# Kernel tuning notes

Hardware: AMD Instinct MI355X
Metric: run time of the kernel (lower is better)

Reference implementation:

```python
import jax, jax.numpy as jnp
import numpy as np

DIM = 256


def setup_inputs() -> dict:
    key = jax.random.key(0)
    ks = jax.random.split(key, 10)
    d = DIM
    inp = {
        "agent": jax.random.normal(ks[0], (64, d), dtype=jnp.float32),
        "x": jax.random.normal(ks[1], (8, 4096, d), dtype=jnp.float32),
        # parameters (stored as [in, out]; y = x @ W + b)
        "W_qkv": jax.random.normal(ks[2], (d, 3 * d), dtype=jnp.float32) * (d ** -0.5),
        "b_qkv": jnp.zeros((3 * d,), dtype=jnp.float32),
        "W_agent": jax.random.normal(ks[3], (d, 2 * d), dtype=jnp.float32) * (d ** -0.5),
        "b_agent": jnp.zeros((2 * d,), dtype=jnp.float32),
        "W_fc1": jax.random.normal(ks[4], (d, d), dtype=jnp.float32) * (d ** -0.5),
        "b_fc1": jnp.zeros((d,), dtype=jnp.float32),
        "W_fc2": jax.random.normal(ks[5], (d, d), dtype=jnp.float32) * (d ** -0.5),
        "b_fc2": jnp.zeros((d,), dtype=jnp.float32),
    }
    return inp


def reference(agent, x, W_qkv, b_qkv, W_agent, b_agent, W_fc1, b_fc1, W_fc2, b_fc2):
    d = x.shape[-1]
    scale = d ** -0.5
    # qkv projection of tokens: [B,N,3d] -> q,k,v each [B,N,d]
    qkv = x @ W_qkv + b_qkv
    q, k, v = jnp.split(qkv, 3, axis=-1)
    # agent projection: [K,2d] -> q_agent,k_agent each [K,d]
    ag = agent @ W_agent + b_agent
    q_agent, k_agent = jnp.split(ag, 2, axis=-1)
    # stage 1: agents attend over tokens -> [B,K,N]
    attn1 = jax.nn.softmax(jnp.einsum('kd,bnd->bkn', q_agent, k) * scale, axis=-1)
    va = jnp.einsum('bkn,bnd->bkd', attn1, v)  # [B,K,d]
    va = va @ W_fc1 + b_fc1
    # stage 2: tokens attend over agents -> [B,N,K]
    attn2 = jax.nn.softmax(jnp.einsum('bnd,kd->bnk', q, k_agent) * scale, axis=-1)
    out = jnp.einsum('bnk,bkd->bnd', attn2, va)  # [B,N,d]
    out = out @ W_fc2 + b_fc2
    return out + x
```

## Files before the change

kernel.cpp:

```cpp
#include <hip/hip_runtime.h>
#include <stdint.h>
#include <string.h>

#define BB 8
#define NN 4096
#define DD 256
#define SCALE 0.0625f

using frag_ab = __attribute__((ext_vector_type(8))) short;
using frag_cd = __attribute__((ext_vector_type(4))) float;

__device__ __forceinline__ unsigned short f2bf(float f) {
    union { float f; unsigned u; } a; a.f = f;
    unsigned r = a.u + 0x7FFFu + ((a.u >> 16) & 1u);
    return (unsigned short)(r >> 16);
}

__global__ __launch_bounds__(256) void k_xprep(
    const float* __restrict__ x, unsigned short* __restrict__ xb,
    unsigned short* __restrict__ xt)
{
    __shared__ float T[64 * 65];
    const int n0 = blockIdx.x * 64, d0 = blockIdx.y * 64, b = blockIdx.z;
    const int tid = threadIdx.x;
#pragma unroll
    for (int p = 0; p < 16; ++p) {
        int idx = p * 256 + tid;
        int n = idx >> 6, d = idx & 63;
        T[n * 65 + d] = x[(size_t)(b * 4096 + n0 + n) * 256 + d0 + d];
    }
    __syncthreads();
#pragma unroll
    for (int p = 0; p < 16; ++p) {
        int idx = p * 256 + tid;
        int n = idx >> 6, d = idx & 63;
        xb[(size_t)(b * 4096 + n0 + n) * 256 + d0 + d] = f2bf(T[n * 65 + d]);
    }
#pragma unroll
    for (int p = 0; p < 16; ++p) {
        int idx = p * 256 + tid;
        int d = idx >> 6, n = idx & 63;
        xt[(size_t)(b * 256 + d0 + d) * 4096 + n0 + n] = f2bf(T[n * 65 + d]);
    }
}

__global__ __launch_bounds__(256) void k_setup1(
    const float* __restrict__ agent, const float* __restrict__ Wag,
    const float* __restrict__ bag, float* __restrict__ ag,
    const float* __restrict__ Wqkv, const float* __restrict__ Wfc1,
    const float* __restrict__ bqkv, const float* __restrict__ bfc1,
    float* __restrict__ T, float* __restrict__ Tb)
{
    __shared__ float sh[256];
    const int bx = blockIdx.x, tid = threadIdx.x;
    if (bx < 64) {
        sh[tid] = agent[bx * 256 + tid];
        __syncthreads();
#pragma unroll
        for (int h = 0; h < 2; ++h) {
            int j = tid + h * 256;
            float s = bag[j];
            for (int kk = 0; kk < 256; ++kk) s += sh[kk] * Wag[kk * 512 + j];
            ag[bx * 512 + j] = s;
        }
    } else {
        const int i = bx - 64;
        sh[tid] = Wqkv[i * 768 + 512 + tid];
        __syncthreads();
        float s = 0.f;
        for (int o = 0; o < 256; ++o) s += sh[o] * Wfc1[o * 256 + tid];
        T[i * 256 + tid] = s;
        if (i == 0) {
            float t = bfc1[tid];
            for (int o = 0; o < 256; ++o) t += bqkv[512 + o] * Wfc1[o * 256 + tid];
            Tb[tid] = t;
        }
    }
}

__global__ __launch_bounds__(256) void k_setup2(
    const float* __restrict__ ag, const float* __restrict__ Wqkv,
    const float* __restrict__ bqkv, unsigned short* __restrict__ P12t,
    float* __restrict__ c12, const float* __restrict__ T,
    const float* __restrict__ Tb, const float* __restrict__ Wfc2,
    float* __restrict__ W3, float* __restrict__ b3)
{
    __shared__ float arow[256];
    __shared__ float red[256];
    const int bx = blockIdx.x, tid = threadIdx.x;
    if (bx < 128) {
        const int c = bx;
        const int woff = (c < 64) ? 256 : 0;
        const int aoff = (c < 64) ? 0 : 256;
        const int row = c & 63;
        arow[tid] = ag[row * 512 + aoff + tid];
        __syncthreads();
        float s = 0.f;
        for (int o = 0; o < 256; ++o) s += Wqkv[tid * 768 + woff + o] * arow[o];
        P12t[(size_t)c * 256 + tid] = f2bf(SCALE * s);
        red[tid] = bqkv[woff + tid] * arow[tid];
        __syncthreads();
        for (int st = 128; st; st >>= 1) {
            if (tid < st) red[tid] += red[tid + st];
            __syncthreads();
        }
        if (tid == 0) c12[c] = SCALE * red[0];
    } else {
        const int i = bx - 128;
        arow[tid] = T[i * 256 + tid];
        __syncthreads();
        float s = 0.f;
        for (int k = 0; k < 256; ++k) s += arow[k] * Wfc2[k * 256 + tid];
        W3[i * 256 + tid] = s;
        if (i == 0) {
            float t = 0.f;
            for (int k = 0; k < 256; ++k) t += Tb[k] * Wfc2[k * 256 + tid];
            b3[tid] = t;
        }
    }
}

__global__ __launch_bounds__(256) void k_logits(
    const unsigned short* __restrict__ xb, const unsigned short* __restrict__ P12t,
    const float* __restrict__ c12, float* __restrict__ l1, float* __restrict__ l2,
    float* __restrict__ statM, float* __restrict__ statS)
{
    __shared__ unsigned short As[64 * 72];
    __shared__ unsigned short Bs[128 * 72];
    const int chunk = blockIdx.x, b = blockIdx.y;
    const int n0 = chunk * 64;
    const int tid = threadIdx.x;
    const int w = tid >> 6, lane = tid & 63;
    const int ml = lane & 15, q = lane >> 4;

    frag_cd acc[4][2];
#pragma unroll
    for (int i = 0; i < 4; ++i)
#pragma unroll
        for (int j = 0; j < 2; ++j)
#pragma unroll
            for (int r = 0; r < 4; ++r) acc[i][j][r] = 0.f;

    for (int kb = 0; kb < 256; kb += 64) {
        __syncthreads();
#pragma unroll
        for (int p = 0; p < 2; ++p) {
            int idx = p * 256 + tid;
            int r = idx >> 3, c = (idx & 7) * 8;
            *(uint4*)&As[r * 72 + c] =
                *(const uint4*)&xb[(size_t)(b * 4096 + n0 + r) * 256 + kb + c];
        }
#pragma unroll
        for (int p = 0; p < 4; ++p) {
            int idx = p * 256 + tid;
            int r = idx >> 3, c = (idx & 7) * 8;
            *(uint4*)&Bs[r * 72 + c] =
                *(const uint4*)&P12t[(size_t)r * 256 + kb + c];
        }
        __syncthreads();
#pragma unroll
        for (int ks = 0; ks < 2; ++ks) {
            const int kk = ks * 32 + q * 8;
            frag_ab a[4], bf[2];
#pragma unroll
            for (int i = 0; i < 4; ++i)
                a[i] = *(const frag_ab*)&As[(i * 16 + ml) * 72 + kk];
#pragma unroll
            for (int j = 0; j < 2; ++j)
                bf[j] = *(const frag_ab*)&Bs[(w * 32 + j * 16 + ml) * 72 + kk];
#pragma unroll
            for (int i = 0; i < 4; ++i)
#pragma unroll
                for (int j = 0; j < 2; ++j)
                    acc[i][j] = __builtin_amdgcn_mfma_f32_16x16x32_bf16(
                        a[i], bf[j], acc[i][j], 0, 0, 0);
        }
    }

    float cc[2];
#pragma unroll
    for (int j = 0; j < 2; ++j) cc[j] = c12[w * 32 + j * 16 + ml];

    if (w < 2) {
#pragma unroll
        for (int j = 0; j < 2; ++j) {
            const int agc = w * 32 + j * 16 + ml;
            float l[4][4];
            float m = -INFINITY;
#pragma unroll
            for (int i = 0; i < 4; ++i)
#pragma unroll
                for (int r = 0; r < 4; ++r) {
                    l[i][r] = acc[i][j][r] + cc[j];
                    m = fmaxf(m, l[i][r]);
                }
            m = fmaxf(m, __shfl_xor(m, 16));
            m = fmaxf(m, __shfl_xor(m, 32));
            float s = 0.f;
#pragma unroll
            for (int i = 0; i < 4; ++i)
#pragma unroll
                for (int r = 0; r < 4; ++r) s += __expf(l[i][r] - m);
            s += __shfl_xor(s, 16);
            s += __shfl_xor(s, 32);
            if (q == 0) {
                size_t si = (size_t)(b * 64 + agc) * 64 + chunk;
                statM[si] = m;
                statS[si] = s;
            }
#pragma unroll
            for (int i = 0; i < 4; ++i)
                *(float4*)&l1[(size_t)(b * 64 + agc) * 4096 + n0 + i * 16 + q * 4] =
                    make_float4(l[i][0], l[i][1], l[i][2], l[i][3]);
        }
    } else {
#pragma unroll
        for (int j = 0; j < 2; ++j) {
            const int agc = (w - 2) * 32 + j * 16 + ml;
#pragma unroll
            for (int i = 0; i < 4; ++i)
#pragma unroll
                for (int r = 0; r < 4; ++r)
                    l2[(size_t)(b * 4096 + n0 + i * 16 + q * 4 + r) * 64 + agc] =
                        acc[i][j][r] + cc[j];
        }
    }
}

__global__ __launch_bounds__(256) void k_va_fused(
    const float* __restrict__ l1, const float* __restrict__ statM,
    const float* __restrict__ statS, const unsigned short* __restrict__ xt,
    float* __restrict__ part)
{
    __shared__ unsigned short As[64 * 144];
    __shared__ unsigned short Bs[128 * 144];
    __shared__ float rowM[64], rowInv[64];
    const int s = blockIdx.x, dh = blockIdx.y, b = blockIdx.z;
    const int tid = threadIdx.x;
    const int w = tid >> 6, lane = tid & 63;
    const int ml = lane & 15, q = lane >> 4;

    if (tid < 64) {
        const float* pm = &statM[(size_t)(b * 64 + tid) * 64];
        const float* ps = &statS[(size_t)(b * 64 + tid) * 64];
        float m = -INFINITY;
#pragma unroll 8
        for (int c = 0; c < 64; ++c) m = fmaxf(m, pm[c]);
        float sum = 0.f;
#pragma unroll 8
        for (int c = 0; c < 64; ++c) sum += ps[c] * __expf(pm[c] - m);
        rowM[tid] = m;
        rowInv[tid] = 1.f / sum;
    }
#pragma unroll
    for (int p = 0; p < 8; ++p) {
        int idx = p * 256 + tid;
        int r = idx >> 4, c = (idx & 15) * 8;
        *(uint4*)&Bs[r * 144 + c] =
            *(const uint4*)&xt[(size_t)(b * 256 + dh * 128 + r) * 4096 + s * 128 + c];
    }
    __syncthreads();
#pragma unroll
    for (int p = 0; p < 32; ++p) {
        int idx = p * 256 + tid;
        int agc = idx >> 7, t = idx & 127;
        float l = l1[(size_t)(b * 64 + agc) * 4096 + s * 128 + t];
        As[agc * 144 + t] = f2bf(__expf(l - rowM[agc]) * rowInv[agc]);
    }
    __syncthreads();

    frag_cd acc[4][2];
#pragma unroll
    for (int i = 0; i < 4; ++i)
#pragma unroll
        for (int j = 0; j < 2; ++j)
#pragma unroll
            for (int r = 0; r < 4; ++r) acc[i][j][r] = 0.f;
#pragma unroll
    for (int ks = 0; ks < 4; ++ks) {
        const int kk = ks * 32 + q * 8;
        frag_ab a[4];
#pragma unroll
        for (int i = 0; i < 4; ++i)
            a[i] = *(const frag_ab*)&As[(i * 16 + ml) * 144 + kk];
#pragma unroll
        for (int j = 0; j < 2; ++j) {
            frag_ab bf = *(const frag_ab*)&Bs[(w * 32 + j * 16 + ml) * 144 + kk];
#pragma unroll
            for (int i = 0; i < 4; ++i)
                acc[i][j] = __builtin_amdgcn_mfma_f32_16x16x32_bf16(
                    a[i], bf, acc[i][j], 0, 0, 0);
        }
    }
#pragma unroll
    for (int i = 0; i < 4; ++i)
#pragma unroll
        for (int j = 0; j < 2; ++j) {
            int d = dh * 128 + w * 32 + j * 16 + ml;
#pragma unroll
            for (int r = 0; r < 4; ++r)
                part[(size_t)((s * 8 + b) * 64 + i * 16 + q * 4 + r) * 256 + d] =
                    acc[i][j][r];
        }
}

__global__ __launch_bounds__(256) void k_fc(
    const float* __restrict__ part, const float* __restrict__ W3,
    const float* __restrict__ b3, unsigned short* __restrict__ va3t)
{
    __shared__ float rowb[256];
    const int row = blockIdx.x, tid = threadIdx.x;
    const int b = row >> 6, agc = row & 63;
    float sv = 0.f;
    for (int s = 0; s < 32; ++s)
        sv += part[(size_t)((s * 8 + b) * 64 + agc) * 256 + tid];
    rowb[tid] = sv;
    __syncthreads();
    float s2 = b3[tid];
    for (int k = 0; k < 256; ++k) s2 += rowb[k] * W3[k * 256 + tid];
    va3t[(size_t)(b * 256 + tid) * 64 + agc] = f2bf(s2);
}

__global__ __launch_bounds__(256) void k_stage2(
    const float* __restrict__ l2, const unsigned short* __restrict__ va3t,
    const float* __restrict__ x, const float* __restrict__ bfc2,
    float* __restrict__ out)
{
    __shared__ unsigned short Ps[64 * 72];
    __shared__ unsigned short Vs[256 * 72];
    const int n0 = blockIdx.x * 64, b = blockIdx.y;
    const int tid = threadIdx.x;
    const int w = tid >> 6, lane = tid & 63;
    const int ml = lane & 15, q = lane >> 4;

#pragma unroll
    for (int p = 0; p < 8; ++p) {
        int idx = p * 256 + tid;
        int r = idx >> 3, c = (idx & 7) * 8;
        *(uint4*)&Vs[r * 72 + c] =
            *(const uint4*)&va3t[(size_t)(b * 256 + r) * 64 + c];
    }

    {
        const int r = tid >> 2, c4 = tid & 3;
        const float* lp = &l2[(size_t)(b * 4096 + n0 + r) * 64 + c4 * 16];
        float v[16];
#pragma unroll
        for (int p = 0; p < 4; ++p) {
            float4 f = *(const float4*)&lp[p * 4];
            v[p * 4 + 0] = f.x; v[p * 4 + 1] = f.y;
            v[p * 4 + 2] = f.z; v[p * 4 + 3] = f.w;
        }
        float m = -INFINITY;
#pragma unroll
        for (int i = 0; i < 16; ++i) m = fmaxf(m, v[i]);
        m = fmaxf(m, __shfl_xor(m, 1));
        m = fmaxf(m, __shfl_xor(m, 2));
        float s = 0.f;
#pragma unroll
        for (int i = 0; i < 16; ++i) { v[i] = __expf(v[i] - m); s += v[i]; }
        s += __shfl_xor(s, 1);
        s += __shfl_xor(s, 2);
        float inv = 1.f / s;
        union { unsigned short u[16]; uint4 vec[2]; } pk;
#pragma unroll
        for (int i = 0; i < 16; ++i) pk.u[i] = f2bf(v[i] * inv);
        *(uint4*)&Ps[r * 72 + c4 * 16] = pk.vec[0];
        *(uint4*)&Ps[r * 72 + c4 * 16 + 8] = pk.vec[1];
    }
    __syncthreads();

    frag_cd acc[4][4];
#pragma unroll
    for (int i = 0; i < 4; ++i)
#pragma unroll
        for (int j = 0; j < 4; ++j)
#pragma unroll
            for (int r = 0; r < 4; ++r) acc[i][j][r] = 0.f;
#pragma unroll
    for (int ks = 0; ks < 2; ++ks) {
        const int kk = ks * 32 + q * 8;
        frag_ab bf[4];
#pragma unroll
        for (int j = 0; j < 4; ++j)
            bf[j] = *(const frag_ab*)&Vs[(w * 64 + j * 16 + ml) * 72 + kk];
#pragma unroll
        for (int i = 0; i < 4; ++i) {
            frag_ab a = *(const frag_ab*)&Ps[(i * 16 + ml) * 72 + kk];
#pragma unroll
            for (int j = 0; j < 4; ++j)
                acc[i][j] = __builtin_amdgcn_mfma_f32_16x16x32_bf16(
                    a, bf[j], acc[i][j], 0, 0, 0);
        }
    }

    float bias[4];
#pragma unroll
    for (int j = 0; j < 4; ++j) bias[j] = bfc2[w * 64 + j * 16 + ml];
#pragma unroll
    for (int i = 0; i < 4; ++i) {
        size_t base = ((size_t)b * 4096 + n0 + i * 16 + q * 4) * 256;
#pragma unroll
        for (int j = 0; j < 4; ++j) {
            int d = w * 64 + j * 16 + ml;
#pragma unroll
            for (int r = 0; r < 4; ++r) {
                size_t a = base + (size_t)r * 256 + d;
                out[a] = acc[i][j][r] + bias[j] + x[a];
            }
        }
    }
}

extern "C" void kernel_launch(void* const* d_in, const int* in_sizes, int n_in,
                              void* d_out, int out_size, void* d_ws, size_t ws_size,
                              hipStream_t stream) {
    const float* agent = (const float*)d_in[0];
    const float* x     = (const float*)d_in[1];
    const float* Wqkv  = (const float*)d_in[2];
    const float* bqkv  = (const float*)d_in[3];
    const float* Wag   = (const float*)d_in[4];
    const float* bag   = (const float*)d_in[5];
    const float* Wfc1  = (const float*)d_in[6];
    const float* bfc1  = (const float*)d_in[7];
    const float* Wfc2  = (const float*)d_in[8];
    const float* bfc2  = (const float*)d_in[9];
    float* out = (float*)d_out;

    char* w = (char*)d_ws;
    size_t off = 0;
    unsigned short* xb   = (unsigned short*)(w + off); off += (size_t)BB * NN * DD * 2;
    unsigned short* xt   = (unsigned short*)(w + off); off += (size_t)BB * DD * NN * 2;
    float* ag   = (float*)(w + off); off += (size_t)64 * 512 * 4;
    float* T    = (float*)(w + off); off += (size_t)256 * 256 * 4;
    float* Tb   = (float*)(w + off); off += 256 * 4;
    unsigned short* P12t = (unsigned short*)(w + off); off += (size_t)128 * 256 * 2;
    float* c12  = (float*)(w + off); off += 128 * 4;
    float* W3   = (float*)(w + off); off += (size_t)256 * 256 * 4;
    float* b3   = (float*)(w + off); off += 256 * 4;
    float* l1   = (float*)(w + off); off += (size_t)BB * 64 * NN * 4;
    float* l2   = (float*)(w + off); off += (size_t)BB * NN * 64 * 4;
    float* statM = (float*)(w + off); off += (size_t)BB * 64 * 64 * 4;
    float* statS = (float*)(w + off); off += (size_t)BB * 64 * 64 * 4;
    float* part = (float*)(w + off); off += (size_t)32 * BB * 64 * 256 * 4;
    unsigned short* va3t = (unsigned short*)(w + off); off += (size_t)BB * DD * 64 * 2;

    k_xprep<<<dim3(64, 4, BB), 256, 0, stream>>>(x, xb, xt);
    k_setup1<<<320, 256, 0, stream>>>(agent, Wag, bag, ag, Wqkv, Wfc1, bqkv, bfc1, T, Tb);
    k_setup2<<<384, 256, 0, stream>>>(ag, Wqkv, bqkv, P12t, c12, T, Tb, Wfc2, W3, b3);
    k_logits<<<dim3(64, BB), 256, 0, stream>>>(xb, P12t, c12, l1, l2, statM, statS);
    k_va_fused<<<dim3(32, 2, BB), 256, 0, stream>>>(l1, statM, statS, xt, part);
    k_fc<<<512, 256, 0, stream>>>(part, W3, b3, va3t);
    k_stage2<<<dim3(64, BB), 256, 0, stream>>>(l2, va3t, x, bfc2, out);
}
```

Before: 187.8 us.

## Fuse x conversion into logits kernel, precompute stage-2 softmax, store partials in bf16

```diff
diff --git a/kernel.cpp b/kernel.cpp
--- a/kernel.cpp
+++ b/kernel.cpp
@@ -6,6 +6,7 @@
 #define NN 4096
 #define DD 256
 #define SCALE 0.0625f
+#define XS 264
 
 using frag_ab = __attribute__((ext_vector_type(8))) short;
 using frag_cd = __attribute__((ext_vector_type(4))) float;
@@ -14,34 +15,6 @@
     union { float f; unsigned u; } a; a.f = f;
     unsigned r = a.u + 0x7FFFu + ((a.u >> 16) & 1u);
     return (unsigned short)(r >> 16);
-}
-
-__global__ __launch_bounds__(256) void k_xprep(
-    const float* __restrict__ x, unsigned short* __restrict__ xb,
-    unsigned short* __restrict__ xt)
-{
-    __shared__ float T[64 * 65];
-    const int n0 = blockIdx.x * 64, d0 = blockIdx.y * 64, b = blockIdx.z;
-    const int tid = threadIdx.x;
-#pragma unroll
-    for (int p = 0; p < 16; ++p) {
-        int idx = p * 256 + tid;
-        int n = idx >> 6, d = idx & 63;
-        T[n * 65 + d] = x[(size_t)(b * 4096 + n0 + n) * 256 + d0 + d];
-    }
-    __syncthreads();
-#pragma unroll
-    for (int p = 0; p < 16; ++p) {
-        int idx = p * 256 + tid;
-        int n = idx >> 6, d = idx & 63;
-        xb[(size_t)(b * 4096 + n0 + n) * 256 + d0 + d] = f2bf(T[n * 65 + d]);
-    }
-#pragma unroll
-    for (int p = 0; p < 16; ++p) {
-        int idx = p * 256 + tid;
-        int d = idx >> 6, n = idx & 63;
-        xt[(size_t)(b * 256 + d0 + d) * 4096 + n0 + n] = f2bf(T[n * 65 + d]);
-    }
 }
 
 __global__ __launch_bounds__(256) void k_setup1(
@@ -120,138 +93,136 @@
     }
 }
 
-__global__ __launch_bounds__(256) void k_logits(
-    const unsigned short* __restrict__ xb, const unsigned short* __restrict__ P12t,
-    const float* __restrict__ c12, float* __restrict__ l1, float* __restrict__ l2,
+__global__ __launch_bounds__(256) void k_xlogits(
+    const float* __restrict__ x, const unsigned short* __restrict__ P12t,
+    const float* __restrict__ c12, unsigned short* __restrict__ xt,
+    float* __restrict__ l1, unsigned short* __restrict__ p2b,
     float* __restrict__ statM, float* __restrict__ statS)
 {
-    __shared__ unsigned short As[64 * 72];
+    __shared__ unsigned short xtile[64 * XS];
     __shared__ unsigned short Bs[128 * 72];
+    __shared__ float Sm[4][64], Ss[4][64], Cm[64];
     const int chunk = blockIdx.x, b = blockIdx.y;
     const int n0 = chunk * 64;
     const int tid = threadIdx.x;
     const int w = tid >> 6, lane = tid & 63;
     const int ml = lane & 15, q = lane >> 4;
 
-    frag_cd acc[4][2];
-#pragma unroll
-    for (int i = 0; i < 4; ++i)
-#pragma unroll
-        for (int j = 0; j < 2; ++j)
-#pragma unroll
-            for (int r = 0; r < 4; ++r) acc[i][j][r] = 0.f;
+#pragma unroll
+    for (int p = 0; p < 16; ++p) {
+        int idx = p * 256 + tid;
+        int tok = idx >> 6, d = (idx & 63) * 4;
+        float4 v = *(const float4*)&x[(size_t)(b * 4096 + n0 + tok) * 256 + d];
+        unsigned short u[4] = {f2bf(v.x), f2bf(v.y), f2bf(v.z), f2bf(v.w)};
+        uint2 pk; memcpy(&pk, u, 8);
+        *(uint2*)&xtile[tok * XS + d] = pk;
+    }
+    __syncthreads();
+#pragma unroll
+    for (int p = 0; p < 16; ++p) {
+        int idx = p * 256 + tid;
+        int d = idx >> 4, seg = idx & 15;
+        unsigned short u[4];
+#pragma unroll
+        for (int k = 0; k < 4; ++k) u[k] = xtile[(seg * 4 + k) * XS + d];
+        uint2 pk; memcpy(&pk, u, 8);
+        *(uint2*)&xt[(size_t)(b * 256 + d) * 4096 + n0 + seg * 4] = pk;
+    }
+
+    frag_cd acc[8];
+#pragma unroll
+    for (int j = 0; j < 8; ++j)
+#pragma unroll
+        for (int r = 0; r < 4; ++r) acc[j][r] = 0.f;
 
     for (int kb = 0; kb < 256; kb += 64) {
         __syncthreads();
-#pragma unroll
-        for (int p = 0; p < 2; ++p) {
-            int idx = p * 256 + tid;
-            int r = idx >> 3, c = (idx & 7) * 8;
-            *(uint4*)&As[r * 72 + c] =
-                *(const uint4*)&xb[(size_t)(b * 4096 + n0 + r) * 256 + kb + c];
-        }
 #pragma unroll
         for (int p = 0; p < 4; ++p) {
             int idx = p * 256 + tid;
             int r = idx >> 3, c = (idx & 7) * 8;
-            *(uint4*)&Bs[r * 72 + c] =
-                *(const uint4*)&P12t[(size_t)r * 256 + kb + c];
+            *(uint4*)&Bs[r * 72 + c] = *(const uint4*)&P12t[(size_t)r * 256 + kb + c];
         }
         __syncthreads();
 #pragma unroll
         for (int ks = 0; ks < 2; ++ks) {
             const int kk = ks * 32 + q * 8;
-            frag_ab a[4], bf[2];
-#pragma unroll
-            for (int i = 0; i < 4; ++i)
-                a[i] = *(const frag_ab*)&As[(i * 16 + ml) * 72 + kk];
-#pragma unroll
-            for (int j = 0; j < 2; ++j)
-                bf[j] = *(const frag_ab*)&Bs[(w * 32 + j * 16 + ml) * 72 + kk];
-#pragma unroll
-            for (int i = 0; i < 4; ++i)
-#pragma unroll
-                for (int j = 0; j < 2; ++j)
-                    acc[i][j] = __builtin_amdgcn_mfma_f32_16x16x32_bf16(
-                        a[i], bf[j], acc[i][j], 0, 0, 0);
-        }
-    }
-
-    float cc[2];
-#pragma unroll
-    for (int j = 0; j < 2; ++j) cc[j] = c12[w * 32 + j * 16 + ml];
-
-    if (w < 2) {
-#pragma unroll
-        for (int j = 0; j < 2; ++j) {
-            const int agc = w * 32 + j * 16 + ml;
-            float l[4][4];
-            float m = -INFINITY;
-#pragma unroll
-            for (int i = 0; i < 4; ++i)
-#pragma unroll
-                for (int r = 0; r < 4; ++r) {
-                    l[i][r] = acc[i][j][r] + cc[j];
-                    m = fmaxf(m, l[i][r]);
-                }
-            m = fmaxf(m, __shfl_xor(m, 16));
-            m = fmaxf(m, __shfl_xor(m, 32));
-            float s = 0.f;
-#pragma unroll
-            for (int i = 0; i < 4; ++i)
-#pragma unroll
-                for (int r = 0; r < 4; ++r) s += __expf(l[i][r] - m);
-            s += __shfl_xor(s, 16);
-            s += __shfl_xor(s, 32);
-            if (q == 0) {
-                size_t si = (size_t)(b * 64 + agc) * 64 + chunk;
-                statM[si] = m;
-                statS[si] = s;
+            frag_ab a = *(const frag_ab*)&xtile[(w * 16 + ml) * XS + kb + kk];
+#pragma unroll
+            for (int j = 0; j < 8; ++j) {
+                frag_ab bf = *(const frag_ab*)&Bs[(j * 16 + ml) * 72 + kk];
+                acc[j] = __builtin_amdgcn_mfma_f32_16x16x32_bf16(a, bf, acc[j], 0, 0, 0);
             }
-#pragma unroll
-            for (int i = 0; i < 4; ++i)
-                *(float4*)&l1[(size_t)(b * 64 + agc) * 4096 + n0 + i * 16 + q * 4] =
-                    make_float4(l[i][0], l[i][1], l[i][2], l[i][3]);
-        }
-    } else {
-#pragma unroll
-        for (int j = 0; j < 2; ++j) {
-            const int agc = (w - 2) * 32 + j * 16 + ml;
-#pragma unroll
-            for (int i = 0; i < 4; ++i)
-#pragma unroll
-                for (int r = 0; r < 4; ++r)
-                    l2[(size_t)(b * 4096 + n0 + i * 16 + q * 4 + r) * 64 + agc] =
-                        acc[i][j][r] + cc[j];
-        }
-    }
-}
-
-__global__ __launch_bounds__(256) void k_va_fused(
+        }
+    }
+
+#pragma unroll
+    for (int j = 0; j < 4; ++j) {
+        *(float4*)&l1[(size_t)(b * 64 + j * 16 + ml) * 4096 + n0 + w * 16 + q * 4] =
+            make_float4(acc[j][0], acc[j][1], acc[j][2], acc[j][3]);
+        float m = fmaxf(fmaxf(acc[j][0], acc[j][1]), fmaxf(acc[j][2], acc[j][3]));
+        m = fmaxf(m, __shfl_xor(m, 16));
+        m = fmaxf(m, __shfl_xor(m, 32));
+        if (q == 0) Sm[w][j * 16 + ml] = m;
+    }
+    __syncthreads();
+    if (tid < 64)
+        Cm[tid] = fmaxf(fmaxf(Sm[0][tid], Sm[1][tid]), fmaxf(Sm[2][tid], Sm[3][tid]));
+    __syncthreads();
+#pragma unroll
+    for (int j = 0; j < 4; ++j) {
+        float cm = Cm[j * 16 + ml];
+        float s = __expf(acc[j][0] - cm) + __expf(acc[j][1] - cm) +
+                  __expf(acc[j][2] - cm) + __expf(acc[j][3] - cm);
+        s += __shfl_xor(s, 16);
+        s += __shfl_xor(s, 32);
+        if (q == 0) Ss[w][j * 16 + ml] = s;
+    }
+    __syncthreads();
+    if (tid < 64) {
+        size_t si = (size_t)(b * 64 + tid) * 64 + chunk;
+        statM[si] = Cm[tid];
+        statS[si] = Ss[0][tid] + Ss[1][tid] + Ss[2][tid] + Ss[3][tid];
+    }
+
+    float v[4][4], cc[4];
+#pragma unroll
+    for (int jj = 0; jj < 4; ++jj) {
+        cc[jj] = c12[64 + jj * 16 + ml];
+#pragma unroll
+        for (int r = 0; r < 4; ++r) v[jj][r] = acc[4 + jj][r] + cc[jj];
+    }
+#pragma unroll
+    for (int r = 0; r < 4; ++r) {
+        float m = fmaxf(fmaxf(v[0][r], v[1][r]), fmaxf(v[2][r], v[3][r]));
+#pragma unroll
+        for (int mask = 1; mask <= 8; mask <<= 1) m = fmaxf(m, __shfl_xor(m, mask));
+        float e[4], s = 0.f;
+#pragma unroll
+        for (int jj = 0; jj < 4; ++jj) { e[jj] = __expf(v[jj][r] - m); s += e[jj]; }
+#pragma unroll
+        for (int mask = 1; mask <= 8; mask <<= 1) s += __shfl_xor(s, mask);
+        float inv = 1.f / s;
+        size_t base = (size_t)(b * 4096 + n0 + w * 16 + q * 4 + r) * 64;
+#pragma unroll
+        for (int jj = 0; jj < 4; ++jj)
+            p2b[base + jj * 16 + ml] = f2bf(e[jj] * inv);
+    }
+}
+
+__global__ __launch_bounds__(256) void k_va(
     const float* __restrict__ l1, const float* __restrict__ statM,
     const float* __restrict__ statS, const unsigned short* __restrict__ xt,
-    float* __restrict__ part)
+    unsigned short* __restrict__ part)
 {
     __shared__ unsigned short As[64 * 144];
     __shared__ unsigned short Bs[128 * 144];
-    __shared__ float rowM[64], rowInv[64];
+    __shared__ float Rm[4][64], Rs[4][64], rowM[64], rowInv[64];
     const int s = blockIdx.x, dh = blockIdx.y, b = blockIdx.z;
     const int tid = threadIdx.x;
     const int w = tid >> 6, lane = tid & 63;
     const int ml = lane & 15, q = lane >> 4;
 
-    if (tid < 64) {
-        const float* pm = &statM[(size_t)(b * 64 + tid) * 64];
-        const float* ps = &statS[(size_t)(b * 64 + tid) * 64];
-        float m = -INFINITY;
-#pragma unroll 8
-        for (int c = 0; c < 64; ++c) m = fmaxf(m, pm[c]);
-        float sum = 0.f;
-#pragma unroll 8
-        for (int c = 0; c < 64; ++c) sum += ps[c] * __expf(pm[c] - m);
-        rowM[tid] = m;
-        rowInv[tid] = 1.f / sum;
-    }
 #pragma unroll
     for (int p = 0; p < 8; ++p) {
         int idx = p * 256 + tid;
@@ -259,13 +230,48 @@
         *(uint4*)&Bs[r * 144 + c] =
             *(const uint4*)&xt[(size_t)(b * 256 + dh * 128 + r) * 4096 + s * 128 + c];
     }
-    __syncthreads();
-#pragma unroll
-    for (int p = 0; p < 32; ++p) {
-        int idx = p * 256 + tid;
-        int agc = idx >> 7, t = idx & 127;
-        float l = l1[(size_t)(b * 64 + agc) * 4096 + s * 128 + t];
-        As[agc * 144 + t] = f2bf(__expf(l - rowM[agc]) * rowInv[agc]);
+
+    const int a = tid & 63, qq = tid >> 6;
+    float pm[16], ps[16];
+    {
+        const float* pmp = &statM[(size_t)(b * 64 + a) * 64 + qq * 16];
+        const float* psp = &statS[(size_t)(b * 64 + a) * 64 + qq * 16];
+#pragma unroll
+        for (int p = 0; p < 4; ++p) {
+            float4 m4 = *(const float4*)&pmp[p * 4];
+            float4 s4 = *(const float4*)&psp[p * 4];
+            pm[p * 4 + 0] = m4.x; pm[p * 4 + 1] = m4.y; pm[p * 4 + 2] = m4.z; pm[p * 4 + 3] = m4.w;
+            ps[p * 4 + 0] = s4.x; ps[p * 4 + 1] = s4.y; ps[p * 4 + 2] = s4.z; ps[p * 4 + 3] = s4.w;
+        }
+        float m = -INFINITY;
+#pragma unroll
+        for (int i = 0; i < 16; ++i) m = fmaxf(m, pm[i]);
+        Rm[qq][a] = m;
+    }
+    __syncthreads();
+    {
+        float M = fmaxf(fmaxf(Rm[0][a], Rm[1][a]), fmaxf(Rm[2][a], Rm[3][a]));
+        float sum = 0.f;
+#pragma unroll
+        for (int i = 0; i < 16; ++i) sum += ps[i] * __expf(pm[i] - M);
+        Rs[qq][a] = sum;
+        if (qq == 0) rowM[a] = M;
+    }
+    __syncthreads();
+    if (tid < 64)
+        rowInv[tid] = 1.f / (Rs[0][tid] + Rs[1][tid] + Rs[2][tid] + Rs[3][tid]);
+    __syncthreads();
+
+#pragma unroll
+    for (int p = 0; p < 8; ++p) {
+        int idx = (p * 256 + tid) * 4;
+        int ag = idx >> 7, t = idx & 127;
+        float4 lv = *(const float4*)&l1[(size_t)(b * 64 + ag) * 4096 + s * 128 + t];
+        float M = rowM[ag], inv = rowInv[ag];
+        unsigned short u[4] = {f2bf(__expf(lv.x - M) * inv), f2bf(__expf(lv.y - M) * inv),
+                               f2bf(__expf(lv.z - M) * inv), f2bf(__expf(lv.w - M) * inv)};
+        uint2 pk; memcpy(&pk, u, 8);
+        *(uint2*)&As[ag * 144 + t] = pk;
     }
     __syncthreads();
 
@@ -279,17 +285,17 @@
 #pragma unroll
     for (int ks = 0; ks < 4; ++ks) {
         const int kk = ks * 32 + q * 8;
-        frag_ab a[4];
+        frag_ab af[4];
 #pragma unroll
         for (int i = 0; i < 4; ++i)
-            a[i] = *(const frag_ab*)&As[(i * 16 + ml) * 144 + kk];
+            af[i] = *(const frag_ab*)&As[(i * 16 + ml) * 144 + kk];
 #pragma unroll
         for (int j = 0; j < 2; ++j) {
             frag_ab bf = *(const frag_ab*)&Bs[(w * 32 + j * 16 + ml) * 144 + kk];
 #pragma unroll
             for (int i = 0; i < 4; ++i)
                 acc[i][j] = __builtin_amdgcn_mfma_f32_16x16x32_bf16(
-                    a[i], bf, acc[i][j], 0, 0, 0);
+                    af[i], bf, acc[i][j], 0, 0, 0);
         }
     }
 #pragma unroll
@@ -300,20 +306,23 @@
 #pragma unroll
             for (int r = 0; r < 4; ++r)
                 part[(size_t)((s * 8 + b) * 64 + i * 16 + q * 4 + r) * 256 + d] =
-                    acc[i][j][r];
+                    f2bf(acc[i][j][r]);
         }
 }
 
 __global__ __launch_bounds__(256) void k_fc(
-    const float* __restrict__ part, const float* __restrict__ W3,
+    const unsigned short* __restrict__ part, const float* __restrict__ W3,
     const float* __restrict__ b3, unsigned short* __restrict__ va3t)
 {
     __shared__ float rowb[256];
     const int row = blockIdx.x, tid = threadIdx.x;
     const int b = row >> 6, agc = row & 63;
     float sv = 0.f;
-    for (int s = 0; s < 32; ++s)
-        sv += part[(size_t)((s * 8 + b) * 64 + agc) * 256 + tid];
+    for (int s = 0; s < 32; ++s) {
+        union { unsigned u; float f; } cv;
+        cv.u = ((unsigned)part[(size_t)((s * 8 + b) * 64 + agc) * 256 + tid]) << 16;
+        sv += cv.f;
+    }
     rowb[tid] = sv;
     __syncthreads();
     float s2 = b3[tid];
@@ -322,7 +331,7 @@
 }
 
 __global__ __launch_bounds__(256) void k_stage2(
-    const float* __restrict__ l2, const unsigned short* __restrict__ va3t,
+    const unsigned short* __restrict__ p2b, const unsigned short* __restrict__ va3t,
     const float* __restrict__ x, const float* __restrict__ bfc2,
     float* __restrict__ out)
 {
@@ -340,33 +349,12 @@
         *(uint4*)&Vs[r * 72 + c] =
             *(const uint4*)&va3t[(size_t)(b * 256 + r) * 64 + c];
     }
-
-    {
-        const int r = tid >> 2, c4 = tid & 3;
-        const float* lp = &l2[(size_t)(b * 4096 + n0 + r) * 64 + c4 * 16];
-        float v[16];
-#pragma unroll
-        for (int p = 0; p < 4; ++p) {
-            float4 f = *(const float4*)&lp[p * 4];
-            v[p * 4 + 0] = f.x; v[p * 4 + 1] = f.y;
-            v[p * 4 + 2] = f.z; v[p * 4 + 3] = f.w;
-        }
-        float m = -INFINITY;
-#pragma unroll
-        for (int i = 0; i < 16; ++i) m = fmaxf(m, v[i]);
-        m = fmaxf(m, __shfl_xor(m, 1));
-        m = fmaxf(m, __shfl_xor(m, 2));
-        float s = 0.f;
-#pragma unroll
-        for (int i = 0; i < 16; ++i) { v[i] = __expf(v[i] - m); s += v[i]; }
-        s += __shfl_xor(s, 1);
-        s += __shfl_xor(s, 2);
-        float inv = 1.f / s;
-        union { unsigned short u[16]; uint4 vec[2]; } pk;
-#pragma unroll
-        for (int i = 0; i < 16; ++i) pk.u[i] = f2bf(v[i] * inv);
-        *(uint4*)&Ps[r * 72 + c4 * 16] = pk.vec[0];
-        *(uint4*)&Ps[r * 72 + c4 * 16 + 8] = pk.vec[1];
+#pragma unroll
+    for (int p = 0; p < 2; ++p) {
+        int idx = p * 256 + tid;
+        int r = idx >> 3, c = (idx & 7) * 8;
+        *(uint4*)&Ps[r * 72 + c] =
+            *(const uint4*)&p2b[(size_t)(b * 4096 + n0 + r) * 64 + c];
     }
     __syncthreads();
 
@@ -405,8 +393,8 @@
             int d = w * 64 + j * 16 + ml;
 #pragma unroll
             for (int r = 0; r < 4; ++r) {
-                size_t a = base + (size_t)r * 256 + d;
-                out[a] = acc[i][j][r] + bias[j] + x[a];
+                size_t ad = base + (size_t)r * 256 + d;
+                out[ad] = acc[i][j][r] + bias[j] + x[ad];
             }
         }
     }
@@ -429,8 +417,10 @@
 
     char* w = (char*)d_ws;
     size_t off = 0;
-    unsigned short* xb   = (unsigned short*)(w + off); off += (size_t)BB * NN * DD * 2;
     unsigned short* xt   = (unsigned short*)(w + off); off += (size_t)BB * DD * NN * 2;
+    float* l1   = (float*)(w + off); off += (size_t)BB * 64 * NN * 4;
+    unsigned short* p2b  = (unsigned short*)(w + off); off += (size_t)BB * NN * 64 * 2;
+    unsigned short* part = (unsigned short*)(w + off); off += (size_t)32 * BB * 64 * 256 * 2;
     float* ag   = (float*)(w + off); off += (size_t)64 * 512 * 4;
     float* T    = (float*)(w + off); off += (size_t)256 * 256 * 4;
     float* Tb   = (float*)(w + off); off += 256 * 4;
@@ -438,18 +428,14 @@
     float* c12  = (float*)(w + off); off += 128 * 4;
     float* W3   = (float*)(w + off); off += (size_t)256 * 256 * 4;
     float* b3   = (float*)(w + off); off += 256 * 4;
-    float* l1   = (float*)(w + off); off += (size_t)BB * 64 * NN * 4;
-    float* l2   = (float*)(w + off); off += (size_t)BB * NN * 64 * 4;
     float* statM = (float*)(w + off); off += (size_t)BB * 64 * 64 * 4;
     float* statS = (float*)(w + off); off += (size_t)BB * 64 * 64 * 4;
-    float* part = (float*)(w + off); off += (size_t)32 * BB * 64 * 256 * 4;
     unsigned short* va3t = (unsigned short*)(w + off); off += (size_t)BB * DD * 64 * 2;
 
-    k_xprep<<<dim3(64, 4, BB), 256, 0, stream>>>(x, xb, xt);
     k_setup1<<<320, 256, 0, stream>>>(agent, Wag, bag, ag, Wqkv, Wfc1, bqkv, bfc1, T, Tb);
     k_setup2<<<384, 256, 0, stream>>>(ag, Wqkv, bqkv, P12t, c12, T, Tb, Wfc2, W3, b3);
-    k_logits<<<dim3(64, BB), 256, 0, stream>>>(xb, P12t, c12, l1, l2, statM, statS);
-    k_va_fused<<<dim3(32, 2, BB), 256, 0, stream>>>(l1, statM, statS, xt, part);
+    k_xlogits<<<dim3(64, BB), 256, 0, stream>>>(x, P12t, c12, xt, l1, p2b, statM, statS);
+    k_va<<<dim3(32, 2, BB), 256, 0, stream>>>(l1, statM, statS, xt, part);
     k_fc<<<512, 256, 0, stream>>>(part, W3, b3, va3t);
-    k_stage2<<<dim3(64, BB), 256, 0, stream>>>(l2, va3t, x, bfc2, out);
-}
+    k_stage2<<<dim3(64, BB), 256, 0, stream>>>(p2b, va3t, x, bfc2, out);
+}
```

Result: faster. 169.3 us (-9.9%).
